# Performance work log

Measured on AMD Instinct MI355X. Metric: run time of the kernel, lower is better.

The kernel has to match this reference:

```python
import math
import jax, jax.numpy as jnp
from jax import lax
import numpy as np

# Defaults of DifferenceOfGaussians
MIN_SIGMA, SIGMA_RATIO, MAX_SIGMA, TRUNCATE = 1.0, 1.2, 10.0, 4.0
K = int(np.log(MAX_SIGMA / MIN_SIGMA) / np.log(SIGMA_RATIO) + 1)  # 13
SIGMAS_NP = np.array([MIN_SIGMA * SIGMA_RATIO ** i for i in range(K + 1)], np.float32)
MAX_RADIUS = int(TRUNCATE * SIGMAS_NP.max() + 0.5)  # 43
THRESHOLD = 0.001
PAD = (3 - 1) // 2  # footprint=3 -> padding 1
MAX_PEAKS = 32768  # fixed cap for jit-compatible nonzero


def _build_pyramid_weight():
    """Replicates GaussianSmoothing kernels (incl. its exp(-(d/(2s))^2) form),
    zero-padded to the common 87x87 support. Shape [K+1, 1, 87, 87] (OIHW)."""
    ksz = 2 * MAX_RADIUS + 1
    W = np.zeros((K + 1, 1, ksz, ksz), np.float32)
    for i, s in enumerate(SIGMAS_NP):
        r = int(TRUNCATE * s + 0.5)
        n = 2 * r + 1
        g = np.arange(n, dtype=np.float32)
        mean = (n - 1) / 2.0
        g1 = (1.0 / (s * math.sqrt(2 * math.pi))) * np.exp(-(((g - mean) / (2.0 * s)) ** 2))
        k2 = np.outer(g1, g1)
        k2 /= k2.sum()
        p = MAX_RADIUS - r
        W[i, 0, p:p + n, p:p + n] = k2
    return jnp.asarray(W)


def setup_inputs() -> dict:
    key = jax.random.key(0)
    x = jax.random.uniform(key, (1, 1, 512, 512), dtype=jnp.float32)
    weight = _build_pyramid_weight()            # [14, 1, 87, 87]
    sigma_list = jnp.asarray(SIGMAS_NP)         # [14]
    return {"x": x, "weight": weight, "sigma_list": sigma_list}


def reference(x, weight, sigma_list):
    # ConstantPad2d(max_radius) then VALID conv -> output spatially == input
    xp = jnp.pad(x, ((0, 0), (0, 0), (MAX_RADIUS, MAX_RADIUS), (MAX_RADIUS, MAX_RADIUS)))
    g = lax.conv_general_dilated(
        xp, weight, window_strides=(1, 1), padding='VALID',
        dimension_numbers=('NCHW', 'OIHW', 'NCHW'))[0]        # [K+1, H, W]
    # DoG stack scaled by sigma: [K, H, W]
    dog = (g[:-1] - g[1:]) * sigma_list[:K][:, None, None]
    # 3D max-pool, kernel 3, stride 1, pad 1 (same shape)
    image_max = lax.reduce_window(dog, -jnp.inf, lax.max,
                                  (3, 3, 3), (1, 1, 1), [(PAD, PAD)] * 3)
    mask = (dog == image_max) & (dog > THRESHOLD)
    # exclude_border: zero out PAD-wide borders along every dim (incl. scale dim)
    mask = mask.at[:PAD].set(False).at[-PAD:].set(False)
    mask = mask.at[:, :PAD].set(False).at[:, -PAD:].set(False)
    mask = mask.at[:, :, :PAD].set(False).at[:, :, -PAD:].set(False)
    # fixed-size nonzero (padded rows have indices (0,0,0); (0,*,*) is always
    # masked out by border exclusion, so real peaks never collide with padding)
    s_idx, y_idx, x_idx = jnp.nonzero(mask, size=MAX_PEAKS, fill_value=0)
    local_maxima = jnp.stack([sigma_list[s_idx],
                              y_idx.astype(jnp.float32),
                              x_idx.astype(jnp.float32)], axis=1)  # [MAX_PEAKS, 3]
    return local_maxima
```

## Files before the change

### kernel.cpp

```cpp
#include <hip/hip_runtime.h>
#include <hip/hip_bf16.h>


#define OFF_H    0
#define OFF_DOG  18350080
#define OFF_BITS 31981568
#define OFF_GCNT 32407552

#define HROWS 640
#define HPAD  43
#define NSIG 13
#define MAXPEAKS 32768

__device__ __forceinline__ void make_w(float s, double sgn, double* wl, int lane) {
    int r = (int)(4.0f * s + 0.5f);
    int n = 2 * r + 1;
    double v0 = 0.0, v1 = 0.0;
    double sd = (double)s;
    if (lane < n) {
        double d = (double)(lane - r), q = d / (2.0 * sd);
        v0 = exp(-q * q);
    }
    if (lane + 64 < n) {
        double d = (double)(lane + 64 - r), q = d / (2.0 * sd);
        v1 = exp(-q * q);
    }
    double part = v0 + v1;
    for (int m = 1; m < 64; m <<= 1) part += __shfl_xor(part, m);
    double inv = sgn / part;
    wl[lane] = v0 * inv;
    if (lane + 64 < 96) wl[lane + 64] = v1 * inv;
}

__global__ __launch_bounds__(256) void hpass(const float* __restrict__ x,
                                             const float* __restrict__ sigma_list,
                                             float* __restrict__ h) {
    const int i = 13 - blockIdx.y;
    const int t = threadIdx.x;
    float s = sigma_list[i];
    int r = (int)(4.0f * s + 0.5f);
    int n = 2 * r + 1;
    int nc8 = (n + 7) & ~7;

    __shared__ double wl[96];
    if (t < 64) make_w(s, +1.0, wl, t);

    {
        float* hp = h + i * (HROWS * 512);
        for (int k = t; k < 688; k += 256) {
            int f = blockIdx.x * 688 + k;
            int g = f >> 9, xc = f & 511;
            int row = (g < HPAD) ? g : (g + 512);
            hp[row * 512 + xc] = 0.0f;
        }
    }

    __shared__ float rowp[8][648];
    int y8 = blockIdx.x * 8;
    for (int rr = 0; rr < 8; ++rr)
        for (int k = t; k < 608; k += 256) {
            int gx = k - 43;
            float val = ((unsigned)gx < 512u) ? x[(y8 + rr) * 512 + gx] : 0.0f;
            rowp[rr][k + (k >> 4)] = val;
        }
    __syncthreads();

    int tsub = t & 31, row = t >> 5;
    int xb = tsub * 16;
    int P0 = 43 - r + xb;
    double acc[16], win[16];
#pragma unroll
    for (int j = 0; j < 16; ++j) acc[j] = 0.0;
#pragma unroll
    for (int sl = 0; sl < 16; ++sl) {
        int p = P0 + sl;
        win[sl] = (double)rowp[row][p + (p >> 4)];
    }
    int full = nc8 & ~15;
    for (int dc = 0; dc < full; dc += 16) {
#pragma unroll
        for (int k = 0; k < 16; ++k) {
            double wd = wl[dc + k];
#pragma unroll
            for (int j = 0; j < 16; ++j)
                acc[j] = fma(wd, win[(k + j) & 15], acc[j]);
            int p = P0 + dc + k + 16;
            win[k] = (double)rowp[row][p + (p >> 4)];
        }
    }
    if (nc8 & 8) {
#pragma unroll
        for (int k = 0; k < 8; ++k) {
            double wd = wl[full + k];
#pragma unroll
            for (int j = 0; j < 16; ++j)
                acc[j] = fma(wd, win[(k + j) & 15], acc[j]);
            int p = P0 + full + k + 16;
            win[k] = (double)rowp[row][p + (p >> 4)];
        }
    }
    float* hp = h + (i * HROWS + HPAD + y8 + row) * 512 + xb;
#pragma unroll
    for (int j = 0; j < 16; ++j) hp[j] = (float)acc[j];
}

__device__ __forceinline__ void conv_acc(const float* __restrict__ bp,
                                         int nc8, const double* __restrict__ wl,
                                         double (&acc)[16]) {
    double win[16];
#pragma unroll
    for (int sl = 0; sl < 16; ++sl) win[sl] = (double)bp[sl * 512];
    int full = nc8 & ~15;
    for (int dc = 0; dc < full; dc += 16) {
        const float* rp = bp + (dc + 16) * 512;
#pragma unroll
        for (int k = 0; k < 16; ++k) {
            double wd = wl[dc + k];
#pragma unroll
            for (int j = 0; j < 16; ++j)
                acc[j] = fma(wd, win[(k + j) & 15], acc[j]);
            win[k] = (double)rp[k * 512];
        }
    }
    if (nc8 & 8) {
        const float* rp = bp + (full + 16) * 512;
#pragma unroll
        for (int k = 0; k < 8; ++k) {
            double wd = wl[full + k];
#pragma unroll
            for (int j = 0; j < 16; ++j)
                acc[j] = fma(wd, win[(k + j) & 15], acc[j]);
            win[k] = (double)rp[k * 512];
        }
    }
}

__global__ __launch_bounds__(64) void vdog(const float* __restrict__ h,
                                           const float* __restrict__ sigma_list,
                                           float* __restrict__ dog) {
    const int di = 12 - blockIdx.z;
    const int lane = threadIdx.x;
    const int x = blockIdx.x * 64 + lane;
    const int y0 = blockIdx.y * 16;
    float s0 = sigma_list[di], s1 = sigma_list[di + 1];
    int r0 = (int)(4.0f * s0 + 0.5f), n0 = 2 * r0 + 1, nc0 = (n0 + 7) & ~7;
    int r1 = (int)(4.0f * s1 + 0.5f), n1 = 2 * r1 + 1, nc1 = (n1 + 7) & ~7;
    __shared__ double wl0[96], wl1[96];
    make_w(s0, +1.0, wl0, lane);
    make_w(s1, -1.0, wl1, lane);
    __syncthreads();
    double acc[16];
#pragma unroll
    for (int j = 0; j < 16; ++j) acc[j] = 0.0;
    const float* hp0 = h + di * (HROWS * 512);
    conv_acc(hp0 + (HPAD + y0 - r0) * 512 + x, nc0, wl0, acc);
    const float* hp1 = hp0 + HROWS * 512;
    conv_acc(hp1 + (HPAD + y0 - r1) * 512 + x, nc1, wl1, acc);
    double sg = (double)s0;
    float* dp = dog + (di * 512 + y0) * 512 + x;
#pragma unroll
    for (int j = 0; j < 16; ++j) dp[j * 512] = (float)(acc[j] * sg);
}

__global__ __launch_bounds__(512) void detect(const float* __restrict__ dog,
                                              unsigned long long* __restrict__ rowbits,
                                              int* __restrict__ gcnt) {
    const int z = blockIdx.y;
    const int sA = 2 * z + 1;
    const bool hasB = (sA < 11);
    const int bx = blockIdx.x;
    const int y0 = bx * 8;
    const int t = threadIdx.x;
    const int w = t >> 6, lane = t & 63;

    if (z == 0) {
        if (t < 64) rowbits[(0 * 512 + y0 + (t >> 3)) * 8 + (t & 7)] = 0ull;
        if (t == 0) gcnt[0 * 64 + bx] = 0;
    } else if (z == 5) {
        if (t < 64) rowbits[(12 * 512 + y0 + (t >> 3)) * 8 + (t & 7)] = 0ull;
        if (t == 0) gcnt[12 * 64 + bx] = 0;
    }

    const int p0 = sA - 1;
    float rm[4][8];
    float vA[8], vB[8];
#pragma unroll
    for (int pp = 0; pp < 4; ++pp) {
        if (pp == 3 && !hasB) {
#pragma unroll
            for (int k = 0; k < 8; ++k) rm[3][k] = -3.0e38f;
        } else {
            const float* dp = dog + (p0 + pp) * (512 * 512) + t;
            float val[10];
#pragma unroll
            for (int q = 0; q < 10; ++q) {
                int yy = y0 - 1 + q;
                val[q] = ((unsigned)yy < 512u) ? dp[yy * 512] : -3.0e38f;
            }
#pragma unroll
            for (int k = 0; k < 8; ++k)
                rm[pp][k] = fmaxf(val[k], fmaxf(val[k + 1], val[k + 2]));
            if (pp == 1) {
#pragma unroll
                for (int k = 0; k < 8; ++k) vA[k] = val[k + 1];
            }
            if (pp == 2) {
#pragma unroll
                for (int k = 0; k < 8; ++k) vB[k] = val[k + 1];
            }
        }
    }

    __shared__ float cml[2][8][512];
    __shared__ int cnt[2][8][8];
#pragma unroll
    for (int k = 0; k < 8; ++k) {
        cml[0][k][t] = fmaxf(rm[0][k], fmaxf(rm[1][k], rm[2][k]));
        cml[1][k][t] = fmaxf(rm[1][k], fmaxf(rm[2][k], rm[3][k]));
    }
    __syncthreads();

#pragma unroll
    for (int k = 0; k < 8; ++k) {
        int y = y0 + k;
        bool peak = false;
        if (t >= 1 && t <= 510 && y >= 1 && y <= 510) {
            float v = vA[k];
            if (v > 0.001f) {
                float mx = fmaxf(cml[0][k][t - 1], fmaxf(cml[0][k][t], cml[0][k][t + 1]));
                peak = (v >= mx);
            }
        }
        unsigned long long m = __ballot(peak);
        if (lane == 0) {
            rowbits[(sA * 512 + y) * 8 + w] = m;
            cnt[0][k][w] = __popcll(m);
        }
    }
    if (hasB) {
        const int sB = sA + 1;
#pragma unroll
        for (int k = 0; k < 8; ++k) {
            int y = y0 + k;
            bool peak = false;
            if (t >= 1 && t <= 510 && y >= 1 && y <= 510) {
                float v = vB[k];
                if (v > 0.001f) {
                    float mx = fmaxf(cml[1][k][t - 1], fmaxf(cml[1][k][t], cml[1][k][t + 1]));
                    peak = (v >= mx);
                }
            }
            unsigned long long m = __ballot(peak);
            if (lane == 0) {
                rowbits[(sB * 512 + y) * 8 + w] = m;
                cnt[1][k][w] = __popcll(m);
            }
        }
    }
    __syncthreads();
    if (t == 0) {
        int c = 0;
#pragma unroll
        for (int k = 0; k < 8; ++k)
#pragma unroll
            for (int q = 0; q < 8; ++q) c += cnt[0][k][q];
        gcnt[sA * 64 + bx] = c;
        if (hasB) {
            c = 0;
#pragma unroll
            for (int k = 0; k < 8; ++k)
#pragma unroll
                for (int q = 0; q < 8; ++q) c += cnt[1][k][q];
            gcnt[(sA + 1) * 64 + bx] = c;
        }
    }
}

__global__ __launch_bounds__(512) void emit(const unsigned long long* __restrict__ rowbits,
                                            const int* __restrict__ gcnt,
                                            const float* __restrict__ sigma_list,
                                            float* __restrict__ out) {
    const int b = blockIdx.x;
    const int s = b >> 6;
    const int y0 = (b & 63) * 8;
    const int t = threadIdx.x;
    const int w = t >> 6, lane = t & 63;

    if (b >= 64 && gcnt[b] == 0) return;

    __shared__ unsigned long long m[64];
    __shared__ int pre[64];
    __shared__ int wsumA[8], wsumB[8];

    if (t < 64) m[t] = rowbits[(s * 512 + y0 + (t >> 3)) * 8 + (t & 7)];

    int pa = 0, pb = 0;
    {
        int c0 = (t < 832) ? gcnt[t] : 0;
        int i1 = t + 512;
        int c1 = (i1 < 832) ? gcnt[i1] : 0;
        pb = c0 + c1;
        if (t < b) pa += c0;
        if (i1 < b) pa += c1;
    }
#pragma unroll
    for (int off = 32; off > 0; off >>= 1) {
        pa += __shfl_down(pa, off);
        pb += __shfl_down(pb, off);
    }
    if (lane == 0) { wsumA[w] = pa; wsumB[w] = pb; }

    if (t < 64) {
        int wc = (int)__popcll(m[t]);
        int inc = wc;
        for (int off = 1; off < 64; off <<= 1) {
            int v = __shfl_up(inc, off);
            if (lane >= off) inc += v;
        }
        pre[t] = inc - wc;
    }
    __syncthreads();

    int gbase = 0, tot = 0;
#pragma unroll
    for (int i = 0; i < 8; ++i) { gbase += wsumA[i]; tot += wsumB[i]; }
    tot = min(tot, MAXPEAKS);

#pragma unroll
    for (int k = 0; k < 8; ++k) {
        int widx = k * 8 + (t >> 6);
        unsigned long long mw = m[widx];
        if ((mw >> lane) & 1ull) {
            int pos = gbase + pre[widx] + (int)__popcll(mw & ((1ull << lane) - 1ull));
            if (pos < MAXPEAKS) {
                out[pos * 3 + 0] = sigma_list[s];
                out[pos * 3 + 1] = (float)(y0 + k);
                out[pos * 3 + 2] = (float)t;
            }
        }
    }

    int idx = b * 512 + t;
    if (idx < MAXPEAKS && idx >= tot) {
        out[idx * 3 + 0] = sigma_list[0];
        out[idx * 3 + 1] = 0.0f;
        out[idx * 3 + 2] = 0.0f;
    }
}

extern "C" void kernel_launch(void* const* d_in, const int* in_sizes, int n_in,
                              void* d_out, int out_size, void* d_ws, size_t ws_size,
                              hipStream_t stream) {
    const float* x     = (const float*)d_in[0];
    const float* sigma = (const float*)d_in[2];
    float* out = (float*)d_out;

    char* ws = (char*)d_ws;
    float* h                     = (float*)(ws + OFF_H);
    float* dog                   = (float*)(ws + OFF_DOG);
    unsigned long long* rowbits  = (unsigned long long*)(ws + OFF_BITS);
    int* gcnt                    = (int*)(ws + OFF_GCNT);

    hpass<<<dim3(64, 14), 256, 0, stream>>>(x, sigma, h);
    vdog<<<dim3(8, 32, 13), 64, 0, stream>>>(h, sigma, dog);
    detect<<<dim3(64, 6), 512, 0, stream>>>(dog, rowbits, gcnt);
    emit<<<832, 512, 0, stream>>>(rowbits, gcnt, sigma, out);
}
```

Baseline: 110.4 us.

## Stage vertical-pass input rows in LDS and split output rows across eight waves

The vertical DoG pass now uses 512-thread blocks covering 32 output rows. Each block first loads the needed horizontal-pass rows for both sigmas into shared memory, then each wave computes 4 output rows from LDS with a 4-deep register window. Previously each 64-thread block computed 16 rows straight from global memory with a 16-deep window. The aim is more parallelism and less redundant global traffic, in exchange for a shorter per-thread window, more rows re-read per output, and large shared-memory use that limits occupancy.

```diff
diff --git a/kernel.cpp b/kernel.cpp
--- a/kernel.cpp
+++ b/kernel.cpp
@@ -104,62 +104,76 @@
     for (int j = 0; j < 16; ++j) hp[j] = (float)acc[j];
 }
 
-__device__ __forceinline__ void conv_acc(const float* __restrict__ bp,
-                                         int nc8, const double* __restrict__ wl,
-                                         double (&acc)[16]) {
-    double win[16];
-#pragma unroll
-    for (int sl = 0; sl < 16; ++sl) win[sl] = (double)bp[sl * 512];
-    int full = nc8 & ~15;
-    for (int dc = 0; dc < full; dc += 16) {
-        const float* rp = bp + (dc + 16) * 512;
-#pragma unroll
-        for (int k = 0; k < 16; ++k) {
-            double wd = wl[dc + k];
-#pragma unroll
-            for (int j = 0; j < 16; ++j)
-                acc[j] = fma(wd, win[(k + j) & 15], acc[j]);
-            win[k] = (double)rp[k * 512];
-        }
-    }
-    if (nc8 & 8) {
-        const float* rp = bp + (full + 16) * 512;
-#pragma unroll
-        for (int k = 0; k < 8; ++k) {
-            double wd = wl[full + k];
-#pragma unroll
-            for (int j = 0; j < 16; ++j)
-                acc[j] = fma(wd, win[(k + j) & 15], acc[j]);
-            win[k] = (double)rp[k * 512];
-        }
-    }
-}
-
-__global__ __launch_bounds__(64) void vdog(const float* __restrict__ h,
-                                           const float* __restrict__ sigma_list,
-                                           float* __restrict__ dog) {
+__global__ __launch_bounds__(512) void vdog(const float* __restrict__ h,
+                                            const float* __restrict__ sigma_list,
+                                            float* __restrict__ dog) {
     const int di = 12 - blockIdx.z;
-    const int lane = threadIdx.x;
-    const int x = blockIdx.x * 64 + lane;
-    const int y0 = blockIdx.y * 16;
+    const int t = threadIdx.x;
+    const int w = t >> 6, lane = t & 63;
+    const int x0 = blockIdx.x * 64;
+    const int y0 = blockIdx.y * 32;
     float s0 = sigma_list[di], s1 = sigma_list[di + 1];
     int r0 = (int)(4.0f * s0 + 0.5f), n0 = 2 * r0 + 1, nc0 = (n0 + 7) & ~7;
     int r1 = (int)(4.0f * s1 + 0.5f), n1 = 2 * r1 + 1, nc1 = (n1 + 7) & ~7;
+
+    __shared__ float ht0[112][64];
+    __shared__ float ht1[120][64];
     __shared__ double wl0[96], wl1[96];
-    make_w(s0, +1.0, wl0, lane);
-    make_w(s1, -1.0, wl1, lane);
-    __syncthreads();
-    double acc[16];
-#pragma unroll
-    for (int j = 0; j < 16; ++j) acc[j] = 0.0;
-    const float* hp0 = h + di * (HROWS * 512);
-    conv_acc(hp0 + (HPAD + y0 - r0) * 512 + x, nc0, wl0, acc);
-    const float* hp1 = hp0 + HROWS * 512;
-    conv_acc(hp1 + (HPAD + y0 - r1) * 512 + x, nc1, wl1, acc);
+
+    if (w == 0) make_w(s0, +1.0, wl0, lane);
+    else if (w == 1) make_w(s1, -1.0, wl1, lane);
+
+    {
+        const float* p0 = h + di * (HROWS * 512) + (HPAD + y0 - r0) * 512 + x0 + lane;
+        int rows0 = nc0 + 32;
+        for (int rr = w; rr < rows0; rr += 8)
+            ht0[rr][lane] = p0[rr * 512];
+        const float* p1 = h + (di + 1) * (HROWS * 512) + (HPAD + y0 - r1) * 512 + x0 + lane;
+        int rows1 = nc1 + 32;
+        for (int rr = w; rr < rows1; rr += 8)
+            ht1[rr][lane] = p1[rr * 512];
+    }
+    __syncthreads();
+
+    double acc[4];
+#pragma unroll
+    for (int jj = 0; jj < 4; ++jj) acc[jj] = 0.0;
+
+    {
+        double win[4];
+#pragma unroll
+        for (int jj = 0; jj < 4; ++jj) win[jj] = (double)ht0[4 * w + jj][lane];
+        for (int kk = 0; kk < nc0; kk += 4) {
+#pragma unroll
+            for (int p = 0; p < 4; ++p) {
+                double wd = wl0[kk + p];
+#pragma unroll
+                for (int jj = 0; jj < 4; ++jj)
+                    acc[jj] = fma(wd, win[(p + jj) & 3], acc[jj]);
+                win[p] = (double)ht0[4 * w + kk + p + 4][lane];
+            }
+        }
+    }
+    {
+        double win[4];
+#pragma unroll
+        for (int jj = 0; jj < 4; ++jj) win[jj] = (double)ht1[4 * w + jj][lane];
+        for (int kk = 0; kk < nc1; kk += 4) {
+#pragma unroll
+            for (int p = 0; p < 4; ++p) {
+                double wd = wl1[kk + p];
+#pragma unroll
+                for (int jj = 0; jj < 4; ++jj)
+                    acc[jj] = fma(wd, win[(p + jj) & 3], acc[jj]);
+                win[p] = (double)ht1[4 * w + kk + p + 4][lane];
+            }
+        }
+    }
+
     double sg = (double)s0;
-    float* dp = dog + (di * 512 + y0) * 512 + x;
-#pragma unroll
-    for (int j = 0; j < 16; ++j) dp[j * 512] = (float)(acc[j] * sg);
+    float* dp = dog + (di * 512 + y0 + 4 * w) * 512 + x0 + lane;
+#pragma unroll
+    for (int jj = 0; jj < 4; ++jj) dp[jj * 512] = (float)(acc[jj] * sg);
 }
 
 __global__ __launch_bounds__(512) void detect(const float* __restrict__ dog,
@@ -362,7 +376,7 @@
     int* gcnt                    = (int*)(ws + OFF_GCNT);
 
     hpass<<<dim3(64, 14), 256, 0, stream>>>(x, sigma, h);
-    vdog<<<dim3(8, 32, 13), 64, 0, stream>>>(h, sigma, dog);
+    vdog<<<dim3(8, 16, 13), 512, 0, stream>>>(h, sigma, dog);
     detect<<<dim3(64, 6), 512, 0, stream>>>(dog, rowbits, gcnt);
     emit<<<832, 512, 0, stream>>>(rowbits, gcnt, sigma, out);
 }
```

New measurement: 115.0 us. 4.1% more time.
